# Kernel optimization log

Hardware: AMD Instinct MI355X
Metric: run time of the kernel (lower is better)

Reference implementation:

```python
import jax, jax.numpy as jnp
import numpy as np

B, N, E, F, C = 4, 10000, 160000, 128, 128
NUM_ITERATIONS = 3  # num_iterations init arg


def setup_inputs() -> dict:
    key = jax.random.key(0)
    ks = jax.random.split(key, 8)
    objects = jax.random.normal(ks[0], (B, N, F), dtype=jnp.float32)
    connections = jax.random.randint(ks[1], (B, E, 2), 0, N, dtype=jnp.int32)
    # small init scales keep exp() in the attention numerically tame (mirrors
    # glorot/orthogonal-scale weights at init)
    object_state_W = jax.random.normal(ks[2], (F, C), dtype=jnp.float32) * (1.0 / np.sqrt(F))
    state_attention_W = jax.random.normal(ks[3], (C, C), dtype=jnp.float32) * 0.05
    linked_state_attention_W = jax.random.normal(ks[4], (C, C), dtype=jnp.float32) * 0.05
    linked_state_W = jax.random.normal(ks[5], (C, C), dtype=jnp.float32) * (1.0 / np.sqrt(C))
    attention_b = jnp.zeros((C,), dtype=jnp.float32)
    state_b = jnp.zeros((C,), dtype=jnp.float32)
    return {
        "objects": objects,
        "object_state_W": object_state_W,
        "state_attention_W": state_attention_W,
        "linked_state_attention_W": linked_state_attention_W,
        "attention_b": attention_b,
        "linked_state_W": linked_state_W,
        "state_b": state_b,
        "connections": connections,
    }


def reference(objects, object_state_W, state_attention_W, linked_state_attention_W,
              attention_b, linked_state_W, state_b, connections):
    # bidirectional: double edges with both orientations  [B, 2E]
    src = jnp.concatenate([connections[:, :, 0], connections[:, :, 1]], axis=1)
    dst = jnp.concatenate([connections[:, :, 1], connections[:, :, 0]], axis=1)

    # initial states: [B, N, C]
    states = jnp.tanh(jnp.einsum('bnf,fc->bnc', objects, object_state_W) + state_b)

    def step_one(states_b, src_b, dst_b):
        # states_b: [N, C]; src_b/dst_b: [2E]
        states_aW = states_b @ state_attention_W          # [N, C]
        linked_aW = states_b @ linked_state_attention_W   # [N, C]
        # per-edge unnormalized attention  [2E, C]
        attention = jnp.exp(states_aW[src_b] + linked_aW[dst_b] + attention_b)
        # scatter-add normalization; self edge contributes 1 (exp(0))
        attention_norm = jnp.ones_like(states_b).at[src_b].add(attention)  # [N, C]
        self_attention = 1.0 / attention_norm
        attention = attention / attention_norm[src_b]
        # weighted neighbor aggregation
        attented = attention * states_b[dst_b]                              # [2E, C]
        linked_gated = jnp.zeros_like(states_b).at[src_b].add(attented)     # [N, C]
        return jnp.tanh(states_b * self_attention + linked_gated @ linked_state_W + state_b)

    step = jax.vmap(step_one)
    for _ in range(NUM_ITERATIONS):
        states = step(states, src, dst)
    return states
```

## Files before the change

kernel.cpp:

```cpp
#include <hip/hip_runtime.h>
#include <hip/hip_bf16.h>


#define BATCH 4
#define NNODE 10000
#define NEDGE 160000
#define TWOE  (2*NEDGE)
#define MROWS (BATCH*NNODE)
#define NCHUNK 64
#define CHUNKE (NEDGE/NCHUNK)
#define PADN  10240
#define EDPAD (TWOE + 8*NNODE)

typedef unsigned short u16;
typedef unsigned int   u32;
typedef __attribute__((ext_vector_type(8))) short bf16x8_t;
typedef __attribute__((ext_vector_type(4))) float f32x4_t;

__device__ __forceinline__ float b2f(u16 h){ return __uint_as_float(((u32)h) << 16); }
__device__ __forceinline__ u16 f2bf(float f){
  u32 u = __float_as_uint(f);
  return (u16)((u + 0x7fffu + ((u >> 16) & 1u)) >> 16);
}
__device__ __forceinline__ float fast_tanh(float x){
  float e = __expf(2.0f * x);
  return fmaf(-2.0f, __builtin_amdgcn_rcpf(e + 1.0f), 1.0f);
}

__global__ void prep_weights(const void* __restrict__ objects,
                             const void* __restrict__ Wo, const void* __restrict__ Wa,
                             const void* __restrict__ Wla, const void* __restrict__ Wl,
                             const void* __restrict__ ab, const void* __restrict__ sb,
                             int* __restrict__ flag, u16* __restrict__ Wt,
                             float* __restrict__ biasf){
  __shared__ int zc, hc;
  if (threadIdx.x == 0){ zc = 0; hc = 0; }
  __syncthreads();
  const u32* objw = (const u32*)objects;
  int z = 0, hcnt = 0;
  for (int i = threadIdx.x; i < 1024; i += 256){
    u32 lo = objw[i] & 0xffffu;
    if (lo == 0) z++;
    if (((lo >> 7) & 0xffu) >= 160u) hcnt++;
  }
  atomicAdd(&zc, z); atomicAdd(&hc, hcnt);
  __syncthreads();
  bool f = (hc > 0 || zc > 512);
  if (blockIdx.x == 0 && threadIdx.x == 0) *flag = f ? 1 : 0;

  int idx = blockIdx.x * 256 + threadIdx.x;
  if (idx < 65536){
    int m = idx >> 14, k = (idx >> 7) & 127, c = idx & 127;
    const void* src = (m == 0) ? Wo : (m == 1) ? Wa : (m == 2) ? Wla : Wl;
    u16 h = f ? f2bf(((const float*)src)[k * 128 + c]) : ((const u16*)src)[k * 128 + c];
    Wt[m * 16384 + c * 128 + k] = h;
  } else {
    int t = idx - 65536;
    const void* src = (t < 128) ? sb : ab;
    int i = t & 127;
    biasf[t] = f ? ((const float*)src)[i] : b2f(((const u16*)src)[i]);
  }
}

__device__ __forceinline__ void chunk_of(int blk, int& b, int& c){
  int xcd = blk & 7;
  b = xcd >> 1;
  c = ((blk >> 3) << 1) | (xcd & 1);
}

__global__ void __launch_bounds__(256) csr_hist(const int* __restrict__ conn,
                                                u16* __restrict__ partial){
  int b, c; chunk_of(blockIdx.x, b, c);
  __shared__ u32 hist[NNODE];
  for (int n = threadIdx.x; n < NNODE; n += 256) hist[n] = 0;
  __syncthreads();
  const int2* cp = (const int2*)conn + (size_t)b * NEDGE + c * CHUNKE;
  for (int i = threadIdx.x; i < CHUNKE; i += 256){
    int2 e = cp[i];
    atomicAdd(&hist[e.x], 1);
    atomicAdd(&hist[e.y], 1);
  }
  __syncthreads();
  u16* prow = partial + (size_t)(b * NCHUNK + c) * PADN;
  for (int n = threadIdx.x; n < NNODE; n += 256) prow[n] = (u16)hist[n];
}

__global__ void __launch_bounds__(256) csr_colscan(u16* __restrict__ partial,
    int* __restrict__ row_start, int* __restrict__ bsum, int* __restrict__ deg){
  int b = blockIdx.x / 40, w = blockIdx.x % 40;
  int n = w * 256 + threadIdx.x;
  u32 run = 0;
  if (n < NNODE){
    #pragma unroll 8
    for (int c = 0; c < NCHUNK; c++){
      size_t idx = (size_t)(b * NCHUNK + c) * PADN + n;
      u32 v = partial[idx];
      partial[idx] = (u16)run;
      run += v;
    }
  }
  u32 pad = (run + 7u) & ~7u;
  __shared__ u32 buf[256];
  buf[threadIdx.x] = pad;
  __syncthreads();
  for (int off = 1; off < 256; off <<= 1){
    u32 x = (threadIdx.x >= (unsigned)off) ? buf[threadIdx.x - off] : 0;
    __syncthreads();
    buf[threadIdx.x] += x;
    __syncthreads();
  }
  u32 incl = buf[threadIdx.x];
  if (n < NNODE){
    row_start[b * (NNODE + 1) + n] = (int)(incl - pad);
    deg[b * NNODE + n] = (int)run;
  }
  if (threadIdx.x == 255) bsum[blockIdx.x] = (int)incl;
}

__global__ void scanC(int* __restrict__ row_start, const int* __restrict__ bsum){
  int b = blockIdx.x / 40, j = blockIdx.x % 40;
  int n = j * 256 + threadIdx.x;
  int off = 0;
  for (int q = b * 40; q < b * 40 + j; q++) off += bsum[q];
  if (n < NNODE) row_start[b * (NNODE + 1) + n] += off;
  if (j == 39 && threadIdx.x == 0)
    row_start[b * (NNODE + 1) + NNODE] = off + bsum[b * 40 + 39];
}

__global__ void __launch_bounds__(256) csr_fill(const int* __restrict__ conn,
    const u16* __restrict__ partial, const int* __restrict__ row_start,
    int* __restrict__ edge_dst){
  int b, c; chunk_of(blockIdx.x, b, c);
  __shared__ u32 cur[NNODE];
  const u16* prow = partial + (size_t)(b * NCHUNK + c) * PADN;
  const int* rs = row_start + b * (NNODE + 1);
  for (int n = threadIdx.x; n < NNODE; n += 256) cur[n] = (u32)rs[n] + prow[n];
  __syncthreads();
  const int2* cp = (const int2*)conn + (size_t)b * NEDGE + c * CHUNKE;
  int* edb = edge_dst + (size_t)b * EDPAD;
  for (int i = threadIdx.x; i < CHUNKE; i += 256){
    int2 e = cp[i];
    u32 p1 = atomicAdd(&cur[e.x], 1); edb[p1] = e.y;
    u32 p2 = atomicAdd(&cur[e.y], 1); edb[p2] = e.x;
  }
}

__global__ void pad_fill(const int* __restrict__ row_start,
                         const int* __restrict__ deg, int* __restrict__ edge_dst,
                         u32* __restrict__ g0, u32* __restrict__ g1){
  if (blockIdx.x == 0){
    size_t base = (size_t)MROWS * 64;
    g0[base + threadIdx.x] = 0;
    g1[base + threadIdx.x] = 0;
  }
  int b = blockIdx.x / 40, j = blockIdx.x % 40;
  int n = j * 256 + threadIdx.x;
  if (n >= NNODE) return;
  const int* rs = row_start + b * (NNODE + 1);
  int s = rs[n] + deg[b * NNODE + n];
  int epad = rs[n + 1];
  int sent = 40000 - 9999 * b;
  int* edb = edge_dst + (size_t)b * EDPAD;
  for (int p = s; p < epad; p++) edb[p] = sent;
}

__device__ __forceinline__ void gemm_tile4(const u16* __restrict__ arow,
    const u16* __restrict__ wt, int lm, int lq, int cofs, f32x4_t acc[4]){
  #pragma unroll
  for (int ks = 0; ks < 4; ks++){
    bf16x8_t a = *(const bf16x8_t*)(arow + ks * 32);
    #pragma unroll
    for (int nb = 0; nb < 4; nb++){
      bf16x8_t bfr = *(const bf16x8_t*)(wt + (cofs + nb * 16 + lm) * 128 + ks * 32 + lq * 8);
      acc[nb] = __builtin_amdgcn_mfma_f32_16x16x32_bf16(a, bfr, acc[nb], 0, 0, 0);
    }
  }
}

__device__ __forceinline__ void gemm_tile4_packed(const u32* __restrict__ Lrow,
    const u16* __restrict__ wt, int lm, int lq, int cofs, f32x4_t acc[4]){
  #pragma unroll
  for (int ks = 0; ks < 4; ks++){
    uint4 wa = *(const uint4*)(Lrow + ks * 32 + lq * 8);
    uint4 wb = *(const uint4*)(Lrow + ks * 32 + lq * 8 + 4);
    bf16x8_t a;
    a[0] = (short)wa.x; a[1] = (short)wa.y; a[2] = (short)wa.z; a[3] = (short)wa.w;
    a[4] = (short)wb.x; a[5] = (short)wb.y; a[6] = (short)wb.z; a[7] = (short)wb.w;
    #pragma unroll
    for (int nb = 0; nb < 4; nb++){
      bf16x8_t bfr = *(const bf16x8_t*)(wt + (cofs + nb * 16 + lm) * 128 + ks * 32 + lq * 8);
      acc[nb] = __builtin_amdgcn_mfma_f32_16x16x32_bf16(a, bfr, acc[nb], 0, 0, 0);
    }
  }
}

__device__ __forceinline__ void phase2_awlaw4(const u16* __restrict__ ldstile,
    const u16* __restrict__ Wt, const float* __restrict__ biasf,
    int lm, int lq, int cofs, int r0, _Float16* __restrict__ eat,
    u32* __restrict__ ghw){
  const u16* Wta  = Wt + 16384;
  const u16* Wtla = Wt + 32768;
  const u16* ldsrow = ldstile + lm * 136 + lq * 8;
  f32x4_t accA[4], accL[4];
  #pragma unroll
  for (int i = 0; i < 4; i++){ accA[i] = (f32x4_t){0.f,0.f,0.f,0.f}; accL[i] = (f32x4_t){0.f,0.f,0.f,0.f}; }
  #pragma unroll
  for (int ks = 0; ks < 4; ks++){
    bf16x8_t a = *(const bf16x8_t*)(ldsrow + ks * 32);
    #pragma unroll
    for (int nb = 0; nb < 4; nb++){
      bf16x8_t ba = *(const bf16x8_t*)(Wta  + (cofs + nb * 16 + lm) * 128 + ks * 32 + lq * 8);
      bf16x8_t bl = *(const bf16x8_t*)(Wtla + (cofs + nb * 16 + lm) * 128 + ks * 32 + lq * 8);
      accA[nb] = __builtin_amdgcn_mfma_f32_16x16x32_bf16(a, ba, accA[nb], 0, 0, 0);
      accL[nb] = __builtin_amdgcn_mfma_f32_16x16x32_bf16(a, bl, accL[nb], 0, 0, 0);
    }
  }
  #pragma unroll
  for (int nb = 0; nb < 4; nb++){
    int col = cofs + nb * 16 + lm;
    float bb = biasf[128 + col];
    #pragma unroll
    for (int i = 0; i < 4; i++){
      int row = r0 + lq * 4 + i;
      float ea = fminf(__expf(accA[nb][i]), 60000.0f);
      eat[(lq * 4 + i) * 128 + col] = (_Float16)ea;
      _Float16 elh = (_Float16)fminf(__expf(accL[nb][i] + bb), 60000.0f);
      u16 sbf = ldstile[(lq * 4 + i) * 136 + col];
      _Float16 sh = (_Float16)b2f(sbf);
      u32 elu = (u32)(*(const u16*)&elh);
      u32 shu = (u32)(*(const u16*)&sh);
      ghw[(size_t)row * 64 + (col & 63)] = elu | (shu << 16);
    }
  }
}

__device__ __forceinline__ void eah_writeback(const _Float16* __restrict__ eat,
    _Float16* __restrict__ eah, int blk_r0, int tid){
  const uint4* src = (const uint4*)eat;
  uint4* dst = (uint4*)(eah + (size_t)blk_r0 * 128);
  dst[tid]       = src[tid];
  dst[tid + 256] = src[tid + 256];
}

__global__ void __launch_bounds__(256) fused_init(const void* __restrict__ obj_raw,
    const int* __restrict__ flag, const u16* __restrict__ Wt,
    const float* __restrict__ biasf, _Float16* __restrict__ eah,
    u32* __restrict__ gat0, u32* __restrict__ gat1){
  __shared__ u16 lds[2][16 * 136];
  __shared__ _Float16 eat[2][16 * 128];
  const int lane = threadIdx.x & 63, wave = threadIdx.x >> 6;
  const int t = wave >> 1, ch = wave & 1, cofs = ch * 64;
  const int r0 = blockIdx.x * 32 + t * 16;
  const int lm = lane & 15, lq = lane >> 4;
  f32x4_t acc[4];
  #pragma unroll
  for (int i = 0; i < 4; i++) acc[i] = (f32x4_t){0.f, 0.f, 0.f, 0.f};
  if (*flag){
    const float* arow = (const float*)obj_raw + (size_t)(r0 + lm) * 128 + lq * 8;
    #pragma unroll
    for (int ks = 0; ks < 4; ks++){
      float4 fa = *(const float4*)(arow + ks * 32);
      float4 fb = *(const float4*)(arow + ks * 32 + 4);
      bf16x8_t a;
      a[0] = (short)f2bf(fa.x); a[1] = (short)f2bf(fa.y);
      a[2] = (short)f2bf(fa.z); a[3] = (short)f2bf(fa.w);
      a[4] = (short)f2bf(fb.x); a[5] = (short)f2bf(fb.y);
      a[6] = (short)f2bf(fb.z); a[7] = (short)f2bf(fb.w);
      #pragma unroll
      for (int nb = 0; nb < 4; nb++){
        bf16x8_t bfr = *(const bf16x8_t*)(Wt + (cofs + nb * 16 + lm) * 128 + ks * 32 + lq * 8);
        acc[nb] = __builtin_amdgcn_mfma_f32_16x16x32_bf16(a, bfr, acc[nb], 0, 0, 0);
      }
    }
  } else {
    gemm_tile4((const u16*)obj_raw + (size_t)(r0 + lm) * 128 + lq * 8, Wt, lm, lq, cofs, acc);
  }
  #pragma unroll
  for (int nb = 0; nb < 4; nb++){
    int col = cofs + nb * 16 + lm;
    float bb = biasf[col];
    #pragma unroll
    for (int i = 0; i < 4; i++)
      lds[t][(lq * 4 + i) * 136 + col] = f2bf(fast_tanh(acc[nb][i] + bb));
  }
  __syncthreads();
  phase2_awlaw4(&lds[t][0], Wt, biasf, lm, lq, cofs, r0, &eat[t][0], ch ? gat1 : gat0);
  __syncthreads();
  eah_writeback(&eat[0][0], eah, blockIdx.x * 32, threadIdx.x);
}

__global__ void __launch_bounds__(256) fused_mid(const u32* __restrict__ lgsa,
    const u16* __restrict__ Wt, const float* __restrict__ biasf,
    _Float16* __restrict__ eah, u32* __restrict__ gat0, u32* __restrict__ gat1){
  __shared__ u16 lds[2][16 * 136];
  __shared__ _Float16 eat[2][16 * 128];
  const int lane = threadIdx.x & 63, wave = threadIdx.x >> 6;
  const int t = wave >> 1, ch = wave & 1, cofs = ch * 64;
  const int r0 = blockIdx.x * 32 + t * 16;
  const int lm = lane & 15, lq = lane >> 4;
  f32x4_t acc[4];
  #pragma unroll
  for (int i = 0; i < 4; i++) acc[i] = (f32x4_t){0.f, 0.f, 0.f, 0.f};
  gemm_tile4_packed(lgsa + (size_t)(r0 + lm) * 128, Wt + 49152, lm, lq, cofs, acc);
  #pragma unroll
  for (int nb = 0; nb < 4; nb++){
    int col = cofs + nb * 16 + lm;
    float bb = biasf[col];
    #pragma unroll
    for (int i = 0; i < 4; i++){
      int row = r0 + lq * 4 + i;
      u32 v = lgsa[(size_t)row * 128 + col];
      u16 hb = (u16)(v >> 16);
      float sa = (float)(*(const _Float16*)&hb);
      lds[t][(lq * 4 + i) * 136 + col] = f2bf(fast_tanh(sa + acc[nb][i] + bb));
    }
  }
  __syncthreads();
  phase2_awlaw4(&lds[t][0], Wt, biasf, lm, lq, cofs, r0, &eat[t][0], ch ? gat1 : gat0);
  __syncthreads();
  eah_writeback(&eat[0][0], eah, blockIdx.x * 32, threadIdx.x);
}

__global__ void __launch_bounds__(256) final_out(const u32* __restrict__ lgsa,
    const u16* __restrict__ Wt, const float* __restrict__ biasf,
    const int* __restrict__ flag, void* __restrict__ outp){
  const int lane = threadIdx.x & 63, wave = threadIdx.x >> 6;
  const int t = wave >> 1, ch = wave & 1, cofs = ch * 64;
  const int r0 = blockIdx.x * 32 + t * 16;
  const int lm = lane & 15, lq = lane >> 4;
  bool f32out = (*flag != 0);
  f32x4_t acc[4];
  #pragma unroll
  for (int i = 0; i < 4; i++) acc[i] = (f32x4_t){0.f, 0.f, 0.f, 0.f};
  gemm_tile4_packed(lgsa + (size_t)(r0 + lm) * 128, Wt + 49152, lm, lq, cofs, acc);
  #pragma unroll
  for (int nb = 0; nb < 4; nb++){
    int col = cofs + nb * 16 + lm;
    float bb = biasf[col];
    #pragma unroll
    for (int i = 0; i < 4; i++){
      int row = r0 + lq * 4 + i;
      u32 vv = lgsa[(size_t)row * 128 + col];
      u16 hb = (u16)(vv >> 16);
      float sa = (float)(*(const _Float16*)&hb);
      float v = fast_tanh(sa + acc[nb][i] + bb);
      if (f32out) ((float*)outp)[(size_t)row * 128 + col] = v;
      else        ((u16*)  outp)[(size_t)row * 128 + col] = f2bf(v);
    }
  }
}

__device__ __forceinline__ void acc_mix(u32 g, float one, float& a1, float& a2){
  asm("v_fma_mix_f32 %0, %2, %3, %0 op_sel:[0,0,0] op_sel_hi:[1,0,0]\n\t"
      "v_fma_mix_f32 %1, %2, %2, %1 op_sel:[0,1,0] op_sel_hi:[1,1,0]"
      : "+v"(a1), "+v"(a2)
      : "v"(g), "v"(one));
}

__device__ __forceinline__ u32 gath1(const u32* __restrict__ gh, int d, int c){
  const u32* p = (const u32*)((const char*)gh + ((size_t)(u32)d << 8));
  return p[c];
}

__global__ void __launch_bounds__(128, 8) edge_kernel(const _Float16* __restrict__ eah,
    const u32* __restrict__ gat0, const u32* __restrict__ gat1,
    const int* __restrict__ row_start, const int* __restrict__ edge_dst,
    u32* __restrict__ lgsa){
  int blk = blockIdx.x;
  int xcd = blk & 7;
  int b = xcd >> 1, h = xcd & 1;
  int i = blk >> 3;
  int n = i * 2 + (int)(threadIdx.x >> 6);
  int node = b * NNODE + n;
  int c = threadIdx.x & 63;
  const u32* gh = (h ? gat1 : gat0) + (size_t)b * NNODE * 64;
  int e0 = __builtin_amdgcn_readfirstlane(row_start[b * (NNODE + 1) + n]);
  int e1 = __builtin_amdgcn_readfirstlane(row_start[b * (NNODE + 1) + n + 1]);
  const int* ed = edge_dst + (size_t)b * EDPAD;

  float ea = (float)eah[(size_t)node * 128 + h * 64 + c];
  u32 self = gh[((size_t)n << 6) + c];
  const float one = 1.0f;

  float s1 = 0.f, s2 = 0.f, t1 = 0.f, t2 = 0.f;
  int ng = (e1 - e0) >> 3;
  if (ng){
    int dB[8]; u32 g[8], gn[8];
    int e = e0;
    { const int* ep = ed + e;
      #pragma unroll
      for (int j = 0; j < 8; j++) dB[j] = __builtin_amdgcn_readfirstlane(ep[j]); }
    #pragma unroll
    for (int j = 0; j < 8; j++) g[j] = gath1(gh, dB[j], c);
    e += 8;
    { const int* ep = ed + e;
      #pragma unroll
      for (int j = 0; j < 8; j++) dB[j] = __builtin_amdgcn_readfirstlane(ep[j]); }
    e += 8;
    int k = 1;
    for (; k + 1 < ng; k += 2){
      #pragma unroll
      for (int j = 0; j < 8; j++) gn[j] = gath1(gh, dB[j], c);
      { const int* ep = ed + e;
        #pragma unroll
        for (int j = 0; j < 8; j++) dB[j] = __builtin_amdgcn_readfirstlane(ep[j]); }
      e += 8;
      #pragma unroll
      for (int j = 0; j < 8; j++) acc_mix(g[j], one, (j & 1) ? t1 : s1, (j & 1) ? t2 : s2);
      #pragma unroll
      for (int j = 0; j < 8; j++) g[j] = gath1(gh, dB[j], c);
      { const int* ep = ed + e;
        #pragma unroll
        for (int j = 0; j < 8; j++) dB[j] = __builtin_amdgcn_readfirstlane(ep[j]); }
      e += 8;
      #pragma unroll
      for (int j = 0; j < 8; j++) acc_mix(gn[j], one, (j & 1) ? t1 : s1, (j & 1) ? t2 : s2);
    }
    if (k < ng){
      #pragma unroll
      for (int j = 0; j < 8; j++) gn[j] = gath1(gh, dB[j], c);
      #pragma unroll
      for (int j = 0; j < 8; j++) acc_mix(g[j], one, (j & 1) ? t1 : s1, (j & 1) ? t2 : s2);
      #pragma unroll
      for (int j = 0; j < 8; j++) acc_mix(gn[j], one, (j & 1) ? t1 : s1, (j & 1) ? t2 : s2);
    } else {
      #pragma unroll
      for (int j = 0; j < 8; j++) acc_mix(g[j], one, (j & 1) ? t1 : s1, (j & 1) ? t2 : s2);
    }
  }

  s1 += t1; s2 += t2;
  float inv = __builtin_amdgcn_rcpf(fmaf(ea, s1, 1.0f));
  float lg = ea * s2 * inv;
  u16 hb = (u16)(self >> 16);
  float s_self = (float)(*(const _Float16*)&hb);
  _Float16 hs = (_Float16)(s_self * inv);
  u32 pk = (u32)f2bf(lg) | ((u32)(*(const u16*)&hs) << 16);
  lgsa[(size_t)node * 128 + h * 64 + c] = pk;
}

extern "C" void kernel_launch(void* const* d_in, const int* in_sizes, int n_in,
                              void* d_out, int out_size, void* d_ws, size_t ws_size,
                              hipStream_t stream){
  (void)in_sizes; (void)n_in; (void)ws_size; (void)out_size;
  const void* objects = d_in[0];
  const void* Wo      = d_in[1];
  const void* Wa      = d_in[2];
  const void* Wla     = d_in[3];
  const void* attn_b  = d_in[4];
  const void* Wl      = d_in[5];
  const void* state_b = d_in[6];
  const int*  conn    = (const int*)d_in[7];

  char* base = (char*)d_ws;
  size_t off = 0;
  auto alloc = [&](size_t bytes) -> char* {
    char* p = base + off;
    off = (off + bytes + 255) & ~(size_t)255;
    return p;
  };
  int*      flag      = (int*)     alloc(256);
  u16*      Wt        = (u16*)     alloc((size_t)4 * 16384 * 2);
  float*    biasf     = (float*)   alloc(256 * 4);
  _Float16* eah       = (_Float16*)alloc((size_t)MROWS * 128 * 2);
  u32*      gat0      = (u32*)     alloc((size_t)(MROWS + 4) * 64 * 4);
  u32*      gat1      = (u32*)     alloc((size_t)(MROWS + 4) * 64 * 4);
  u32*      lgsa      = (u32*)     alloc((size_t)MROWS * 128 * 4);
  u16*      partial   = (u16*)     alloc((size_t)BATCH * NCHUNK * PADN * 2);
  int*      row_start = (int*)     alloc((size_t)BATCH * (NNODE + 1) * 4);
  int*      edge_dst  = (int*)     alloc((size_t)BATCH * EDPAD * 4);
  int*      deg       = (int*)     alloc((size_t)MROWS * 4);
  int*      bsum      = (int*)     alloc(160 * 4);

  prep_weights<<<257, 256, 0, stream>>>(objects, Wo, Wa, Wla, Wl, attn_b, state_b,
                                        flag, Wt, biasf);

  csr_hist<<<256, 256, 0, stream>>>(conn, partial);
  csr_colscan<<<160, 256, 0, stream>>>(partial, row_start, bsum, deg);
  scanC<<<160, 256, 0, stream>>>(row_start, bsum);
  csr_fill<<<256, 256, 0, stream>>>(conn, partial, row_start, edge_dst);
  pad_fill<<<160, 256, 0, stream>>>(row_start, deg, edge_dst, gat0, gat1);

  fused_init<<<MROWS / 32, 256, 0, stream>>>(objects, flag, Wt, biasf, eah, gat0, gat1);
  edge_kernel<<<MROWS, 128, 0, stream>>>(eah, gat0, gat1, row_start, edge_dst, lgsa);
  fused_mid<<<MROWS / 32, 256, 0, stream>>>(lgsa, Wt, biasf, eah, gat0, gat1);
  edge_kernel<<<MROWS, 128, 0, stream>>>(eah, gat0, gat1, row_start, edge_dst, lgsa);
  fused_mid<<<MROWS / 32, 256, 0, stream>>>(lgsa, Wt, biasf, eah, gat0, gat1);
  edge_kernel<<<MROWS, 128, 0, stream>>>(eah, gat0, gat1, row_start, edge_dst, lgsa);
  final_out<<<MROWS / 32, 256, 0, stream>>>(lgsa, Wt, biasf, flag, d_out);
}
```

Baseline: 355.9 us.

## Merge split gather tables and have each edge-kernel lane handle two channels

Replaces the two half-channel gather tables with one interleaved table of 128 channels per row. Each lane of the edge kernel now gathers 8 bytes per neighbour (two channels) and handles the whole node, so the grid shrinks by half. Blocks are mapped by batch and node half instead of batch and channel half. This removes the duplicated edge-index reads and loop overhead of processing every node twice. In exchange, each XCD's gather working set per batch doubles, which may hurt L2 hit rates.

Result: slower. 393.0 us (+10.4%).

```diff
diff --git a/kernel.cpp b/kernel.cpp
--- a/kernel.cpp
+++ b/kernel.cpp
@@ -147,11 +147,11 @@
 
 __global__ void pad_fill(const int* __restrict__ row_start,
                          const int* __restrict__ deg, int* __restrict__ edge_dst,
-                         u32* __restrict__ g0, u32* __restrict__ g1){
+                         u32* __restrict__ gat){
   if (blockIdx.x == 0){
-    size_t base = (size_t)MROWS * 64;
-    g0[base + threadIdx.x] = 0;
-    g1[base + threadIdx.x] = 0;
+    size_t base = (size_t)MROWS * 128;
+    gat[base + threadIdx.x]       = 0;
+    gat[base + 256 + threadIdx.x] = 0;
   }
   int b = blockIdx.x / 40, j = blockIdx.x % 40;
   int n = j * 256 + threadIdx.x;
@@ -197,7 +197,7 @@
 __device__ __forceinline__ void phase2_awlaw4(const u16* __restrict__ ldstile,
     const u16* __restrict__ Wt, const float* __restrict__ biasf,
     int lm, int lq, int cofs, int r0, _Float16* __restrict__ eat,
-    u32* __restrict__ ghw){
+    u32* __restrict__ gat){
   const u16* Wta  = Wt + 16384;
   const u16* Wtla = Wt + 32768;
   const u16* ldsrow = ldstile + lm * 136 + lq * 8;
@@ -229,7 +229,7 @@
       _Float16 sh = (_Float16)b2f(sbf);
       u32 elu = (u32)(*(const u16*)&elh);
       u32 shu = (u32)(*(const u16*)&sh);
-      ghw[(size_t)row * 64 + (col & 63)] = elu | (shu << 16);
+      gat[(size_t)row * 128 + col] = elu | (shu << 16);
     }
   }
 }
@@ -245,7 +245,7 @@
 __global__ void __launch_bounds__(256) fused_init(const void* __restrict__ obj_raw,
     const int* __restrict__ flag, const u16* __restrict__ Wt,
     const float* __restrict__ biasf, _Float16* __restrict__ eah,
-    u32* __restrict__ gat0, u32* __restrict__ gat1){
+    u32* __restrict__ gat){
   __shared__ u16 lds[2][16 * 136];
   __shared__ _Float16 eat[2][16 * 128];
   const int lane = threadIdx.x & 63, wave = threadIdx.x >> 6;
@@ -284,14 +284,14 @@
       lds[t][(lq * 4 + i) * 136 + col] = f2bf(fast_tanh(acc[nb][i] + bb));
   }
   __syncthreads();
-  phase2_awlaw4(&lds[t][0], Wt, biasf, lm, lq, cofs, r0, &eat[t][0], ch ? gat1 : gat0);
+  phase2_awlaw4(&lds[t][0], Wt, biasf, lm, lq, cofs, r0, &eat[t][0], gat);
   __syncthreads();
   eah_writeback(&eat[0][0], eah, blockIdx.x * 32, threadIdx.x);
 }
 
 __global__ void __launch_bounds__(256) fused_mid(const u32* __restrict__ lgsa,
     const u16* __restrict__ Wt, const float* __restrict__ biasf,
-    _Float16* __restrict__ eah, u32* __restrict__ gat0, u32* __restrict__ gat1){
+    _Float16* __restrict__ eah, u32* __restrict__ gat){
   __shared__ u16 lds[2][16 * 136];
   __shared__ _Float16 eat[2][16 * 128];
   const int lane = threadIdx.x & 63, wave = threadIdx.x >> 6;
@@ -316,7 +316,7 @@
     }
   }
   __syncthreads();
-  phase2_awlaw4(&lds[t][0], Wt, biasf, lm, lq, cofs, r0, &eat[t][0], ch ? gat1 : gat0);
+  phase2_awlaw4(&lds[t][0], Wt, biasf, lm, lq, cofs, r0, &eat[t][0], gat);
   __syncthreads();
   eah_writeback(&eat[0][0], eah, blockIdx.x * 32, threadIdx.x);
 }
@@ -357,41 +357,44 @@
       : "v"(g), "v"(one));
 }
 
-__device__ __forceinline__ u32 gath1(const u32* __restrict__ gh, int d, int c){
-  const u32* p = (const u32*)((const char*)gh + ((size_t)(u32)d << 8));
-  return p[c];
-}
+__device__ __forceinline__ uint2 gath2(const u32* __restrict__ gat, int d, int c){
+  return *(const uint2*)((const char*)gat + ((size_t)(u32)d << 9) + ((size_t)(u32)(c << 3)));
+}
+
+#define ACC2(G, p) \
+  acc_mix((G).x, one, (p) ? t1x : s1x, (p) ? t2x : s2x); \
+  acc_mix((G).y, one, (p) ? t1y : s1y, (p) ? t2y : s2y);
 
 __global__ void __launch_bounds__(128, 8) edge_kernel(const _Float16* __restrict__ eah,
-    const u32* __restrict__ gat0, const u32* __restrict__ gat1,
-    const int* __restrict__ row_start, const int* __restrict__ edge_dst,
-    u32* __restrict__ lgsa){
+    const u32* __restrict__ gat, const int* __restrict__ row_start,
+    const int* __restrict__ edge_dst, u32* __restrict__ lgsa){
   int blk = blockIdx.x;
   int xcd = blk & 7;
-  int b = xcd >> 1, h = xcd & 1;
+  int b = xcd >> 1, hh = xcd & 1;
   int i = blk >> 3;
-  int n = i * 2 + (int)(threadIdx.x >> 6);
+  int n = hh * 5000 + i * 2 + (int)(threadIdx.x >> 6);
   int node = b * NNODE + n;
   int c = threadIdx.x & 63;
-  const u32* gh = (h ? gat1 : gat0) + (size_t)b * NNODE * 64;
+  const u32* gb = gat + (size_t)b * NNODE * 128;
   int e0 = __builtin_amdgcn_readfirstlane(row_start[b * (NNODE + 1) + n]);
   int e1 = __builtin_amdgcn_readfirstlane(row_start[b * (NNODE + 1) + n + 1]);
   const int* ed = edge_dst + (size_t)b * EDPAD;
 
-  float ea = (float)eah[(size_t)node * 128 + h * 64 + c];
-  u32 self = gh[((size_t)n << 6) + c];
+  u32 eav = ((const u32*)eah)[(size_t)node * 64 + c];
+  uint2 self = gath2(gb, n, c);
   const float one = 1.0f;
 
-  float s1 = 0.f, s2 = 0.f, t1 = 0.f, t2 = 0.f;
+  float s1x=0.f, s2x=0.f, t1x=0.f, t2x=0.f;
+  float s1y=0.f, s2y=0.f, t1y=0.f, t2y=0.f;
   int ng = (e1 - e0) >> 3;
   if (ng){
-    int dB[8]; u32 g[8], gn[8];
+    int dB[8]; uint2 g[8], gn[8];
     int e = e0;
     { const int* ep = ed + e;
       #pragma unroll
       for (int j = 0; j < 8; j++) dB[j] = __builtin_amdgcn_readfirstlane(ep[j]); }
     #pragma unroll
-    for (int j = 0; j < 8; j++) g[j] = gath1(gh, dB[j], c);
+    for (int j = 0; j < 8; j++) g[j] = gath2(gb, dB[j], c);
     e += 8;
     { const int* ep = ed + e;
       #pragma unroll
@@ -400,43 +403,52 @@
     int k = 1;
     for (; k + 1 < ng; k += 2){
       #pragma unroll
-      for (int j = 0; j < 8; j++) gn[j] = gath1(gh, dB[j], c);
+      for (int j = 0; j < 8; j++) gn[j] = gath2(gb, dB[j], c);
       { const int* ep = ed + e;
         #pragma unroll
         for (int j = 0; j < 8; j++) dB[j] = __builtin_amdgcn_readfirstlane(ep[j]); }
       e += 8;
       #pragma unroll
-      for (int j = 0; j < 8; j++) acc_mix(g[j], one, (j & 1) ? t1 : s1, (j & 1) ? t2 : s2);
-      #pragma unroll
-      for (int j = 0; j < 8; j++) g[j] = gath1(gh, dB[j], c);
+      for (int j = 0; j < 8; j++){ ACC2(g[j], j & 1); }
+      #pragma unroll
+      for (int j = 0; j < 8; j++) g[j] = gath2(gb, dB[j], c);
       { const int* ep = ed + e;
         #pragma unroll
         for (int j = 0; j < 8; j++) dB[j] = __builtin_amdgcn_readfirstlane(ep[j]); }
       e += 8;
       #pragma unroll
-      for (int j = 0; j < 8; j++) acc_mix(gn[j], one, (j & 1) ? t1 : s1, (j & 1) ? t2 : s2);
+      for (int j = 0; j < 8; j++){ ACC2(gn[j], j & 1); }
     }
     if (k < ng){
       #pragma unroll
-      for (int j = 0; j < 8; j++) gn[j] = gath1(gh, dB[j], c);
-      #pragma unroll
-      for (int j = 0; j < 8; j++) acc_mix(g[j], one, (j & 1) ? t1 : s1, (j & 1) ? t2 : s2);
-      #pragma unroll
-      for (int j = 0; j < 8; j++) acc_mix(gn[j], one, (j & 1) ? t1 : s1, (j & 1) ? t2 : s2);
+      for (int j = 0; j < 8; j++) gn[j] = gath2(gb, dB[j], c);
+      #pragma unroll
+      for (int j = 0; j < 8; j++){ ACC2(g[j], j & 1); }
+      #pragma unroll
+      for (int j = 0; j < 8; j++){ ACC2(gn[j], j & 1); }
     } else {
       #pragma unroll
-      for (int j = 0; j < 8; j++) acc_mix(g[j], one, (j & 1) ? t1 : s1, (j & 1) ? t2 : s2);
-    }
-  }
-
-  s1 += t1; s2 += t2;
-  float inv = __builtin_amdgcn_rcpf(fmaf(ea, s1, 1.0f));
-  float lg = ea * s2 * inv;
-  u16 hb = (u16)(self >> 16);
-  float s_self = (float)(*(const _Float16*)&hb);
-  _Float16 hs = (_Float16)(s_self * inv);
-  u32 pk = (u32)f2bf(lg) | ((u32)(*(const u16*)&hs) << 16);
-  lgsa[(size_t)node * 128 + h * 64 + c] = pk;
+      for (int j = 0; j < 8; j++){ ACC2(g[j], j & 1); }
+    }
+  }
+
+  s1x += t1x; s2x += t2x; s1y += t1y; s2y += t2y;
+  union { u32 u; _Float16 f[2]; } ec; ec.u = eav;
+  u32 out[2];
+  float S1[2] = {s1x, s1y};
+  float S2[2] = {s2x, s2y};
+  u32 SV[2] = {self.x, self.y};
+  #pragma unroll
+  for (int k2 = 0; k2 < 2; k2++){
+    float ea = (float)ec.f[k2];
+    float inv = __builtin_amdgcn_rcpf(fmaf(ea, S1[k2], 1.0f));
+    float lg = ea * S2[k2] * inv;
+    u16 hb = (u16)(SV[k2] >> 16);
+    float s_self = (float)(*(const _Float16*)&hb);
+    _Float16 hs = (_Float16)(s_self * inv);
+    out[k2] = (u32)f2bf(lg) | ((u32)(*(const u16*)&hs) << 16);
+  }
+  *(uint2*)(lgsa + (size_t)node * 128 + (c << 1)) = *(const uint2*)out;
 }
 
 extern "C" void kernel_launch(void* const* d_in, const int* in_sizes, int n_in,
@@ -463,8 +475,7 @@
   u16*      Wt        = (u16*)     alloc((size_t)4 * 16384 * 2);
   float*    biasf     = (float*)   alloc(256 * 4);
   _Float16* eah       = (_Float16*)alloc((size_t)MROWS * 128 * 2);
-  u32*      gat0      = (u32*)     alloc((size_t)(MROWS + 4) * 64 * 4);
-  u32*      gat1      = (u32*)     alloc((size_t)(MROWS + 4) * 64 * 4);
+  u32*      gat       = (u32*)     alloc((size_t)(MROWS + 4) * 128 * 4);
   u32*      lgsa      = (u32*)     alloc((size_t)MROWS * 128 * 4);
   u16*      partial   = (u16*)     alloc((size_t)BATCH * NCHUNK * PADN * 2);
   int*      row_start = (int*)     alloc((size_t)BATCH * (NNODE + 1) * 4);
@@ -479,13 +490,13 @@
   csr_colscan<<<160, 256, 0, stream>>>(partial, row_start, bsum, deg);
   scanC<<<160, 256, 0, stream>>>(row_start, bsum);
   csr_fill<<<256, 256, 0, stream>>>(conn, partial, row_start, edge_dst);
-  pad_fill<<<160, 256, 0, stream>>>(row_start, deg, edge_dst, gat0, gat1);
-
-  fused_init<<<MROWS / 32, 256, 0, stream>>>(objects, flag, Wt, biasf, eah, gat0, gat1);
-  edge_kernel<<<MROWS, 128, 0, stream>>>(eah, gat0, gat1, row_start, edge_dst, lgsa);
-  fused_mid<<<MROWS / 32, 256, 0, stream>>>(lgsa, Wt, biasf, eah, gat0, gat1);
-  edge_kernel<<<MROWS, 128, 0, stream>>>(eah, gat0, gat1, row_start, edge_dst, lgsa);
-  fused_mid<<<MROWS / 32, 256, 0, stream>>>(lgsa, Wt, biasf, eah, gat0, gat1);
-  edge_kernel<<<MROWS, 128, 0, stream>>>(eah, gat0, gat1, row_start, edge_dst, lgsa);
+  pad_fill<<<160, 256, 0, stream>>>(row_start, deg, edge_dst, gat);
+
+  fused_init<<<MROWS / 32, 256, 0, stream>>>(objects, flag, Wt, biasf, eah, gat);
+  edge_kernel<<<MROWS / 2, 128, 0, stream>>>(eah, gat, row_start, edge_dst, lgsa);
+  fused_mid<<<MROWS / 32, 256, 0, stream>>>(lgsa, Wt, biasf, eah, gat);
+  edge_kernel<<<MROWS / 2, 128, 0, stream>>>(eah, gat, row_start, edge_dst, lgsa);
+  fused_mid<<<MROWS / 32, 256, 0, stream>>>(lgsa, Wt, biasf, eah, gat);
+  edge_kernel<<<MROWS / 2, 128, 0, stream>>>(eah, gat, row_start, edge_dst, lgsa);
   final_out<<<MROWS / 32, 256, 0, stream>>>(lgsa, Wt, biasf, flag, d_out);
 }
```

## Process two nodes per wavefront in edge kernel to interleave gathers

Applied to the files above, without the earlier changes.

Each wavefront in the edge aggregation kernel now handles two consecutive nodes and interleaves their index loads, gathers and accumulations. The aim is more independent memory requests in flight per wave, hiding gather latency. The grid is halved and launch bounds are lowered to allow more registers. pad_fill also writes sentinels into the tail beyond the last row, because the software-pipelined loop may prefetch indices past a node's range. The cost is higher register pressure and lower occupancy, and imbalance when the two nodes have very different degrees.

Result: no change. 356.2 us (+0.1%).

```diff
diff --git a/kernel.cpp b/kernel.cpp
--- a/kernel.cpp
+++ b/kernel.cpp
@@ -154,13 +154,17 @@
     g1[base + threadIdx.x] = 0;
   }
   int b = blockIdx.x / 40, j = blockIdx.x % 40;
+  const int* rs = row_start + b * (NNODE + 1);
+  int sent = 40000 - 9999 * b;
+  int* edb = edge_dst + (size_t)b * EDPAD;
+  if (j == 0){
+    int T = rs[NNODE];
+    for (int p = T + (int)threadIdx.x; p < EDPAD; p += 256) edb[p] = sent;
+  }
   int n = j * 256 + threadIdx.x;
   if (n >= NNODE) return;
-  const int* rs = row_start + b * (NNODE + 1);
   int s = rs[n] + deg[b * NNODE + n];
   int epad = rs[n + 1];
-  int sent = 40000 - 9999 * b;
-  int* edb = edge_dst + (size_t)b * EDPAD;
   for (int p = s; p < epad; p++) edb[p] = sent;
 }
 
@@ -362,7 +366,14 @@
   return p[c];
 }
 
-__global__ void __launch_bounds__(128, 8) edge_kernel(const _Float16* __restrict__ eah,
+#define LDIDX(d, p) { const int* ep_ = (p); _Pragma("unroll") \
+  for (int j = 0; j < 8; j++) d[j] = __builtin_amdgcn_readfirstlane(ep_[j]); }
+#define GATH8(g, d) { _Pragma("unroll") \
+  for (int j = 0; j < 8; j++) g[j] = gath1(gh, d[j], c); }
+#define CONS8(g, s1, s2, t1, t2) { _Pragma("unroll") \
+  for (int j = 0; j < 8; j++) acc_mix(g[j], one, (j & 1) ? t1 : s1, (j & 1) ? t2 : s2); }
+
+__global__ void __launch_bounds__(128, 6) edge_kernel(const _Float16* __restrict__ eah,
     const u32* __restrict__ gat0, const u32* __restrict__ gat1,
     const int* __restrict__ row_start, const int* __restrict__ edge_dst,
     u32* __restrict__ lgsa){
@@ -370,73 +381,98 @@
   int xcd = blk & 7;
   int b = xcd >> 1, h = xcd & 1;
   int i = blk >> 3;
-  int n = i * 2 + (int)(threadIdx.x >> 6);
-  int node = b * NNODE + n;
+  int w = (int)(threadIdx.x >> 6);
+  int nA = i * 4 + w * 2, nB = nA + 1;
   int c = threadIdx.x & 63;
   const u32* gh = (h ? gat1 : gat0) + (size_t)b * NNODE * 64;
-  int e0 = __builtin_amdgcn_readfirstlane(row_start[b * (NNODE + 1) + n]);
-  int e1 = __builtin_amdgcn_readfirstlane(row_start[b * (NNODE + 1) + n + 1]);
+  const int* rs = row_start + b * (NNODE + 1);
+  int eA  = __builtin_amdgcn_readfirstlane(rs[nA]);
+  int eA1 = __builtin_amdgcn_readfirstlane(rs[nA + 1]);
+  int eB1 = __builtin_amdgcn_readfirstlane(rs[nB + 1]);
+  int eB = eA1;
   const int* ed = edge_dst + (size_t)b * EDPAD;
 
-  float ea = (float)eah[(size_t)node * 128 + h * 64 + c];
-  u32 self = gh[((size_t)n << 6) + c];
+  float eaA = (float)eah[(size_t)(b * NNODE + nA) * 128 + h * 64 + c];
+  float eaB = (float)eah[(size_t)(b * NNODE + nB) * 128 + h * 64 + c];
+  u32 selfA = gh[((size_t)nA << 6) + c];
+  u32 selfB = gh[((size_t)nB << 6) + c];
   const float one = 1.0f;
 
-  float s1 = 0.f, s2 = 0.f, t1 = 0.f, t2 = 0.f;
-  int ng = (e1 - e0) >> 3;
-  if (ng){
-    int dB[8]; u32 g[8], gn[8];
-    int e = e0;
-    { const int* ep = ed + e;
-      #pragma unroll
-      for (int j = 0; j < 8; j++) dB[j] = __builtin_amdgcn_readfirstlane(ep[j]); }
-    #pragma unroll
-    for (int j = 0; j < 8; j++) g[j] = gath1(gh, dB[j], c);
-    e += 8;
-    { const int* ep = ed + e;
-      #pragma unroll
-      for (int j = 0; j < 8; j++) dB[j] = __builtin_amdgcn_readfirstlane(ep[j]); }
-    e += 8;
-    int k = 1;
-    for (; k + 1 < ng; k += 2){
-      #pragma unroll
-      for (int j = 0; j < 8; j++) gn[j] = gath1(gh, dB[j], c);
-      { const int* ep = ed + e;
-        #pragma unroll
-        for (int j = 0; j < 8; j++) dB[j] = __builtin_amdgcn_readfirstlane(ep[j]); }
-      e += 8;
-      #pragma unroll
-      for (int j = 0; j < 8; j++) acc_mix(g[j], one, (j & 1) ? t1 : s1, (j & 1) ? t2 : s2);
-      #pragma unroll
-      for (int j = 0; j < 8; j++) g[j] = gath1(gh, dB[j], c);
-      { const int* ep = ed + e;
-        #pragma unroll
-        for (int j = 0; j < 8; j++) dB[j] = __builtin_amdgcn_readfirstlane(ep[j]); }
-      e += 8;
-      #pragma unroll
-      for (int j = 0; j < 8; j++) acc_mix(gn[j], one, (j & 1) ? t1 : s1, (j & 1) ? t2 : s2);
-    }
-    if (k < ng){
-      #pragma unroll
-      for (int j = 0; j < 8; j++) gn[j] = gath1(gh, dB[j], c);
-      #pragma unroll
-      for (int j = 0; j < 8; j++) acc_mix(g[j], one, (j & 1) ? t1 : s1, (j & 1) ? t2 : s2);
-      #pragma unroll
-      for (int j = 0; j < 8; j++) acc_mix(gn[j], one, (j & 1) ? t1 : s1, (j & 1) ? t2 : s2);
-    } else {
-      #pragma unroll
-      for (int j = 0; j < 8; j++) acc_mix(g[j], one, (j & 1) ? t1 : s1, (j & 1) ? t2 : s2);
-    }
-  }
-
-  s1 += t1; s2 += t2;
-  float inv = __builtin_amdgcn_rcpf(fmaf(ea, s1, 1.0f));
-  float lg = ea * s2 * inv;
-  u16 hb = (u16)(self >> 16);
-  float s_self = (float)(*(const _Float16*)&hb);
-  _Float16 hs = (_Float16)(s_self * inv);
-  u32 pk = (u32)f2bf(lg) | ((u32)(*(const u16*)&hs) << 16);
-  lgsa[(size_t)node * 128 + h * 64 + c] = pk;
+  float sA1=0.f, sA2=0.f, tA1=0.f, tA2=0.f;
+  float sB1=0.f, sB2=0.f, tB1=0.f, tB2=0.f;
+  int ngA = (eA1 - eA) >> 3, ngB = (eB1 - eB) >> 3;
+  int dA[8], dB[8]; u32 gA[8], gB[8], hA[8], hB[8];
+
+  if (ngA){ LDIDX(dA, ed + eA); }
+  if (ngB){ LDIDX(dB, ed + eB); }
+  if (ngA){ GATH8(gA, dA); eA += 8; LDIDX(dA, ed + eA); }
+  if (ngB){ GATH8(gB, dB); eB += 8; LDIDX(dB, ed + eB); }
+
+  int m = ngA < ngB ? ngA : ngB;
+  int cons = 0;
+  for (; cons + 2 <= m; cons += 2){
+    GATH8(hA, dA); eA += 8; LDIDX(dA, ed + eA);
+    GATH8(hB, dB); eB += 8; LDIDX(dB, ed + eB);
+    CONS8(gA, sA1, sA2, tA1, tA2);
+    CONS8(gB, sB1, sB2, tB1, tB2);
+    GATH8(gA, dA); eA += 8; LDIDX(dA, ed + eA);
+    GATH8(gB, dB); eB += 8; LDIDX(dB, ed + eB);
+    CONS8(hA, sA1, sA2, tA1, tA2);
+    CONS8(hB, sB1, sB2, tB1, tB2);
+  }
+
+  { int rem = ngA - cons;
+    if (rem > 0){
+      int k = 1;
+      for (; k + 1 < rem; k += 2){
+        GATH8(hA, dA); eA += 8; LDIDX(dA, ed + eA);
+        CONS8(gA, sA1, sA2, tA1, tA2);
+        GATH8(gA, dA); eA += 8; LDIDX(dA, ed + eA);
+        CONS8(hA, sA1, sA2, tA1, tA2);
+      }
+      if (k < rem){
+        GATH8(hA, dA);
+        CONS8(gA, sA1, sA2, tA1, tA2);
+        CONS8(hA, sA1, sA2, tA1, tA2);
+      } else {
+        CONS8(gA, sA1, sA2, tA1, tA2);
+      }
+    }
+  }
+  { int rem = ngB - cons;
+    if (rem > 0){
+      int k = 1;
+      for (; k + 1 < rem; k += 2){
+        GATH8(hB, dB); eB += 8; LDIDX(dB, ed + eB);
+        CONS8(gB, sB1, sB2, tB1, tB2);
+        GATH8(gB, dB); eB += 8; LDIDX(dB, ed + eB);
+        CONS8(hB, sB1, sB2, tB1, tB2);
+      }
+      if (k < rem){
+        GATH8(hB, dB);
+        CONS8(gB, sB1, sB2, tB1, tB2);
+        CONS8(hB, sB1, sB2, tB1, tB2);
+      } else {
+        CONS8(gB, sB1, sB2, tB1, tB2);
+      }
+    }
+  }
+
+  sA1 += tA1; sA2 += tA2; sB1 += tB1; sB2 += tB2;
+  { float inv = __builtin_amdgcn_rcpf(fmaf(eaA, sA1, 1.0f));
+    float lg = eaA * sA2 * inv;
+    u16 hb = (u16)(selfA >> 16);
+    float s_self = (float)(*(const _Float16*)&hb);
+    _Float16 hs = (_Float16)(s_self * inv);
+    u32 pk = (u32)f2bf(lg) | ((u32)(*(const u16*)&hs) << 16);
+    lgsa[(size_t)(b * NNODE + nA) * 128 + h * 64 + c] = pk; }
+  { float inv = __builtin_amdgcn_rcpf(fmaf(eaB, sB1, 1.0f));
+    float lg = eaB * sB2 * inv;
+    u16 hb = (u16)(selfB >> 16);
+    float s_self = (float)(*(const _Float16*)&hb);
+    _Float16 hs = (_Float16)(s_self * inv);
+    u32 pk = (u32)f2bf(lg) | ((u32)(*(const u16*)&hs) << 16);
+    lgsa[(size_t)(b * NNODE + nB) * 128 + h * 64 + c] = pk; }
 }
 
 extern "C" void kernel_launch(void* const* d_in, const int* in_sizes, int n_in,
@@ -482,10 +518,10 @@
   pad_fill<<<160, 256, 0, stream>>>(row_start, deg, edge_dst, gat0, gat1);
 
   fused_init<<<MROWS / 32, 256, 0, stream>>>(objects, flag, Wt, biasf, eah, gat0, gat1);
-  edge_kernel<<<MROWS, 128, 0, stream>>>(eah, gat0, gat1, row_start, edge_dst, lgsa);
+  edge_kernel<<<MROWS / 2, 128, 0, stream>>>(eah, gat0, gat1, row_start, edge_dst, lgsa);
   fused_mid<<<MROWS / 32, 256, 0, stream>>>(lgsa, Wt, biasf, eah, gat0, gat1);
-  edge_kernel<<<MROWS, 128, 0, stream>>>(eah, gat0, gat1, row_start, edge_dst, lgsa);
+  edge_kernel<<<MROWS / 2, 128, 0, stream>>>(eah, gat0, gat1, row_start, edge_dst, lgsa);
   fused_mid<<<MROWS / 32, 256, 0, stream>>>(lgsa, Wt, biasf, eah, gat0, gat1);
-  edge_kernel<<<MROWS, 128, 0, stream>>>(eah, gat0, gat1, row_start, edge_dst, lgsa);
+  edge_kernel<<<MROWS / 2, 128, 0, stream>>>(eah, gat0, gat1, row_start, edge_dst, lgsa);
   final_out<<<MROWS / 32, 256, 0, stream>>>(lgsa, Wt, biasf, flag, d_out);
 }
```
